# Kernel optimization log

Measured on AMD Instinct MI355X. Metric: run time of the kernel, lower is better.

The kernel has to match this reference:

```python
import jax, jax.numpy as jnp
import numpy as np

D = 64        # inner_feature_len (dim)
HID = 128     # hidden_channels of the edge MLP
NCONV = 2     # n_conv
STEPS = 3     # Set2Set processing_steps
NSEG = 128    # number of graphs in the batch


def setup_inputs() -> dict:
    key = jax.random.key(0)
    ks = jax.random.split(key, 30)
    N, E, FN, FE = 10000, 64000, 92, 41
    s = 0.05
    p = lambda i, shape: jax.random.normal(ks[i], shape, jnp.float32) * s
    return {
        "x": jax.random.normal(ks[0], (N, FN), jnp.float32),
        "edge_attr": jax.random.uniform(ks[1], (E, FE), dtype=jnp.float32),
        "lin0_w": p(2, (D, FN)), "lin0_b": p(3, (D,)),
        "nn1_w": p(4, (HID, FE)), "nn1_b": p(5, (HID,)),
        "nn2_w": p(6, (D * D, HID)), "nn2_b": p(7, (D * D,)),
        "root_w": p(8, (D, D)), "conv_b": p(9, (D,)),
        "gru_w_ih": p(10, (3 * D, D)), "gru_w_hh": p(11, (3 * D, D)),
        "gru_b_ih": p(12, (3 * D,)), "gru_b_hh": p(13, (3 * D,)),
        "lstm_w_ih": p(14, (4 * D, 2 * D)), "lstm_w_hh": p(15, (4 * D, D)),
        "lstm_b_ih": p(16, (4 * D,)), "lstm_b_hh": p(17, (4 * D,)),
        "lin1_w": p(18, (D, 2 * D)), "lin1_b": p(19, (D,)),
        "lin2_w": p(20, (1, D)), "lin2_b": p(21, (1,)),
        "edge_index": jax.random.randint(ks[22], (2, E), 0, N, dtype=jnp.int32),
        "batch": jnp.sort(jax.random.randint(ks[23], (N,), 0, NSEG, dtype=jnp.int32)),
    }


def _gru_step(m, h, w_ih, w_hh, b_ih, b_hh):
    # torch GRU gate order: r, z, n
    gi = m @ w_ih.T + b_ih
    gh = h @ w_hh.T + b_hh
    r = jax.nn.sigmoid(gi[:, :D] + gh[:, :D])
    z = jax.nn.sigmoid(gi[:, D:2 * D] + gh[:, D:2 * D])
    n = jnp.tanh(gi[:, 2 * D:] + r * gh[:, 2 * D:])
    return (1.0 - z) * n + z * h


def _forward(x, edge_attr, lin0_w, lin0_b, nn1_w, nn1_b, nn2_w, nn2_b, root_w, conv_b,
             gru_w_ih, gru_w_hh, gru_b_ih, gru_b_hh, lstm_w_ih, lstm_w_hh, lstm_b_ih,
             lstm_b_hh, lin1_w, lin1_b, lin2_w, lin2_b, edge_index, batch):
    N = x.shape[0]
    src, dst = edge_index[0], edge_index[1]

    # Edge-conditioned weight matrices: [E, D, D] (dominant intermediate)
    We = (jax.nn.relu(edge_attr @ nn1_w.T + nn1_b) @ nn2_w.T + nn2_b).reshape(-1, D, D)
    deg = jnp.clip(jax.ops.segment_sum(jnp.ones_like(src, jnp.float32), dst, num_segments=N), 1.0, None)

    out = jax.nn.relu(x @ lin0_w.T + lin0_b)   # [N, D]
    h = out                                     # GRU hidden (num_layers=1)
    for _ in range(NCONV):
        # NNConv: gather -> per-edge matmul -> scatter-mean, plus root transform + bias
        msg = jnp.einsum('ei,eio->eo', out[src], We)                 # [E, D]
        agg = jax.ops.segment_sum(msg, dst, num_segments=N) / deg[:, None]
        m = jax.nn.relu(agg + out @ root_w.T + conv_b)
        h = _gru_step(m, h, gru_w_ih, gru_w_hh, gru_b_ih, gru_b_hh)
        out = h

    # Set2Set pooling (LSTM-attention readout)
    q_star = jnp.zeros((NSEG, 2 * D), x.dtype)
    hl = jnp.zeros((NSEG, D), x.dtype)
    cl = jnp.zeros((NSEG, D), x.dtype)
    for _ in range(STEPS):
        g = q_star @ lstm_w_ih.T + lstm_b_ih + hl @ lstm_w_hh.T + lstm_b_hh
        i = jax.nn.sigmoid(g[:, :D])
        f = jax.nn.sigmoid(g[:, D:2 * D])
        gg = jnp.tanh(g[:, 2 * D:3 * D])
        o = jax.nn.sigmoid(g[:, 3 * D:])
        cl = f * cl + i * gg
        hl = o * jnp.tanh(cl)
        q = hl                                   # [NSEG, D]
        e = jnp.sum(out * q[batch], axis=-1)     # [N]
        mmax = jax.ops.segment_max(e, batch, num_segments=NSEG)
        a = jnp.exp(e - mmax[batch])
        denom = jax.ops.segment_sum(a, batch, num_segments=NSEG)
        a = a / denom[batch]
        r = jax.ops.segment_sum(a[:, None] * out, batch, num_segments=NSEG)  # [NSEG, D]
        q_star = jnp.concatenate([q, r], axis=1)

    y = jax.nn.relu(q_star @ lin1_w.T + lin1_b) @ lin2_w.T + lin2_b
    return y.reshape(-1)


def reference(x, edge_attr, lin0_w, lin0_b, nn1_w, nn1_b, nn2_w, nn2_b, root_w, conv_b,
              gru_w_ih, gru_w_hh, gru_b_ih, gru_b_hh, lstm_w_ih, lstm_w_hh, lstm_b_ih,
              lstm_b_hh, lin1_w, lin1_b, lin2_w, lin2_b, edge_index, batch):
    return _forward(x, edge_attr, lin0_w, lin0_b, nn1_w, nn1_b, nn2_w, nn2_b, root_w,
                    conv_b, gru_w_ih, gru_w_hh, gru_b_ih, gru_b_hh, lstm_w_ih, lstm_w_hh,
                    lstm_b_ih, lstm_b_hh, lin1_w, lin1_b, lin2_w, lin2_b, edge_index, batch)
```

## Files before the change

kernel.cpp:

```cpp
#include <hip/hip_runtime.h>
#include <hip/hip_bf16.h>
#include <math.h>

#define DD 64
#define HIDC 128
#define FN 92
#define FE 41
#define S2CAP 192

typedef unsigned short u16;
typedef short bf16x8 __attribute__((ext_vector_type(8)));
typedef float f32x4 __attribute__((ext_vector_type(4)));
typedef u16 u16x8 __attribute__((ext_vector_type(8)));

__device__ __forceinline__ float sigmoidf_(float x){ return 1.f/(1.f+expf(-x)); }

__device__ __forceinline__ u16 f2bf(float v){
  union { float f; unsigned u; } x; x.f = v;
  unsigned r = x.u + 0x7fff + ((x.u >> 16) & 1);
  return (u16)(r >> 16);
}
__device__ __forceinline__ float bf2f(u16 v){
  union { float f; unsigned u; } x; x.u = ((unsigned)v) << 16;
  return x.f;
}
__device__ __forceinline__ void split_bf(float v, u16& h, u16& l){
  h = f2bf(v); l = f2bf(v - bf2f(h));
}

__global__ void k_pack(const float* __restrict__ lin0_w, const float* __restrict__ nn1_w,
                       const float* __restrict__ root_w, const float* __restrict__ gwih,
                       const float* __restrict__ gwhh, const float* __restrict__ lwih,
                       const float* __restrict__ lwhh, const float* __restrict__ lin1_w,
                       float* __restrict__ lin0T, float* __restrict__ nn1T,
                       float* __restrict__ rootT, float* __restrict__ wihT,
                       float* __restrict__ whhT, float* __restrict__ lwihT,
                       float* __restrict__ lwhhT, float* __restrict__ lin1T)
{
  int idx = blockIdx.x*blockDim.x + threadIdx.x;
  if (idx < 92*64){ int k=idx/64, o=idx%64; lin0T[k*64+o] = lin0_w[o*92+k]; return; } idx -= 92*64;
  if (idx < 41*128){ int k=idx/128, h=idx%128; nn1T[k*128+h] = nn1_w[h*41+k]; return; } idx -= 41*128;
  if (idx < 64*64){ int i=idx/64, o=idx%64; rootT[i*64+o] = root_w[o*64+i]; return; } idx -= 64*64;
  if (idx < 64*192){ int i=idx/192, g=idx%192; wihT[i*192+g] = gwih[g*64+i]; return; } idx -= 64*192;
  if (idx < 64*192){ int i=idx/192, g=idx%192; whhT[i*192+g] = gwhh[g*64+i]; return; } idx -= 64*192;
  if (idx < 128*256){ int j=idx/256, t=idx%256; lwihT[j*256+t] = lwih[t*128+j]; return; } idx -= 128*256;
  if (idx < 64*256){ int j=idx/256, t=idx%256; lwhhT[j*256+t] = lwhh[t*64+j]; return; } idx -= 64*256;
  if (idx < 128*64){ int j=idx/64, t=idx%64; lin1T[j*64+t] = lin1_w[t*128+j]; return; }
}

__global__ void k_pack_b2(const float* __restrict__ nn2_w,
                          u16* __restrict__ BhT, u16* __restrict__ BlT){
  int idx = blockIdx.x*256 + threadIdx.x;
  if (idx >= 524288) return;
  int i  = idx & 63;
  int ho = (idx >> 6) & 4095;
  int c  = idx >> 18;
  int h = ho >> 6, o = ho & 63;
  float v = nn2_w[(size_t)(i*64+o)*128 + c*64 + h];
  u16 hi, lo; split_bf(v, hi, lo);
  BhT[idx] = hi; BlT[idx] = lo;
}

__global__ void k_pack_b1(const float* __restrict__ nn1_w,
                          u16* __restrict__ BT1h, u16* __restrict__ BT1l){
  int idx = blockIdx.x*256 + threadIdx.x;
  if (idx >= 8192) return;
  int h = idx >> 6, k = idx & 63;
  float v = (k < FE) ? nn1_w[(size_t)h*FE + k] : 0.f;
  u16 hi, lo; split_bf(v, hi, lo);
  BT1h[idx] = hi; BT1l[idx] = lo;
}

__global__ void k_split_ea(const float* __restrict__ ea, const int* __restrict__ sortedE,
                           u16* __restrict__ eaH, u16* __restrict__ eaL, int E){
  int idx = blockIdx.x*256 + threadIdx.x;
  if (idx >= E*64) return;
  int ew = idx >> 6, k = idx & 63;
  int e = sortedE[ew];
  float v = (k < FE) ? ea[(size_t)e*FE + k] : 0.f;
  u16 hi, lo; split_bf(v, hi, lo);
  eaH[idx] = hi; eaL[idx] = lo;
}

__global__ __launch_bounds__(256) void k_node_mlp(const float* __restrict__ x,
    const float* __restrict__ lin0T, const float* __restrict__ lin0_b,
    const float* __restrict__ nn2_b,
    float* __restrict__ out, u16* __restrict__ outH, u16* __restrict__ outL,
    float* __restrict__ bterm, int N)
{
  __shared__ float xs[16][FN];
  const int w = threadIdx.x>>6, o = threadIdx.x&63;
  const int nb = blockIdx.x*16 + w*4;
  for (int idx = o; idx < 4*FN; idx += 64){
    int j = idx/FN, k = idx%FN;
    int n = nb + j;
    xs[w*4+j][k] = (n<N) ? x[(size_t)n*FN + k] : 0.f;
  }
  float acc[4];
  float bv = lin0_b[o];
  #pragma unroll
  for (int j=0;j<4;j++) acc[j] = bv;
  for (int k=0;k<FN;k++){
    float lw = lin0T[k*64+o];
    #pragma unroll
    for (int j=0;j<4;j++) acc[j] = fmaf(xs[w*4+j][k], lw, acc[j]);
  }
  float v[4];
  #pragma unroll
  for (int j=0;j<4;j++){
    v[j] = fmaxf(acc[j], 0.f);
    int n = nb + j;
    if (n < N){
      out[(size_t)n*64+o] = v[j];
      u16 hi, lo; split_bf(v[j], hi, lo);
      outH[(size_t)n*64+o] = hi;
      outL[(size_t)n*64+o] = lo;
    }
  }
  float bt[4] = {0.f,0.f,0.f,0.f};
  for (int i=0;i<64;i++){
    float wnb = nn2_b[i*64+o];
    #pragma unroll
    for (int j=0;j<4;j++) bt[j] = fmaf(__shfl(v[j], i, 64), wnb, bt[j]);
  }
  #pragma unroll
  for (int j=0;j<4;j++){
    int n = nb + j;
    if (n < N) bterm[(size_t)n*64+o] = bt[j];
  }
}

__global__ void k_count(const int* __restrict__ dst, const int* __restrict__ src,
                        float* __restrict__ deg, int* __restrict__ scnt, int E){
  int e = blockIdx.x*blockDim.x + threadIdx.x;
  if (e < E){
    atomicAdd(&deg[dst[e]], 1.f);
    atomicAdd(&scnt[src[e]], 1);
  }
}

__global__ void k_scan1(const int* __restrict__ cnt, int* __restrict__ excl,
                        int* __restrict__ bsum, int N){
  __shared__ int buf[256];
  int i = blockIdx.x*256 + threadIdx.x;
  int v = (i<N) ? cnt[i] : 0;
  buf[threadIdx.x] = v;
  __syncthreads();
  #pragma unroll
  for (int off=1; off<256; off<<=1){
    int t = (threadIdx.x>=off) ? buf[threadIdx.x-off] : 0;
    __syncthreads();
    buf[threadIdx.x] += t;
    __syncthreads();
  }
  if (i<N) excl[i] = buf[threadIdx.x] - v;
  if (threadIdx.x==255) bsum[blockIdx.x] = buf[255];
}
__global__ void k_scan2(int* __restrict__ bsum, int nb){
  __shared__ int buf[256];
  int v = (threadIdx.x<nb) ? bsum[threadIdx.x] : 0;
  buf[threadIdx.x] = v;
  __syncthreads();
  #pragma unroll
  for (int off=1; off<256; off<<=1){
    int t = (threadIdx.x>=off) ? buf[threadIdx.x-off] : 0;
    __syncthreads();
    buf[threadIdx.x] += t;
    __syncthreads();
  }
  if (threadIdx.x<nb) bsum[threadIdx.x] = buf[threadIdx.x] - v;
}
__global__ void k_scan3(int* __restrict__ starts, int* __restrict__ cursor,
                        const int* __restrict__ bsum, int N, int E){
  int i = blockIdx.x*256 + threadIdx.x;
  if (i<N){
    int s = starts[i] + bsum[blockIdx.x];
    starts[i] = s;
    cursor[i] = s;
  }
  if (i==0) starts[N] = E;
}

__global__ void k_sort(const int* __restrict__ src, const int* __restrict__ dst,
                       int* __restrict__ cursor, int* __restrict__ sortedE,
                       int* __restrict__ dstS, int E){
  int e = blockIdx.x*256 + threadIdx.x;
  if (e < E){
    int s = src[e];
    int p = atomicAdd(&cursor[s], 1);
    sortedE[p] = e;
    dstS[p] = dst[e];
  }
}

__global__ __launch_bounds__(256,3) void k_edge_mlp_mfma(
    const u16* __restrict__ eaH, const u16* __restrict__ eaL,
    const u16* __restrict__ BT1h, const u16* __restrict__ BT1l,
    const float* __restrict__ nn1_b, float* __restrict__ hidden, int E)
{
  const int lane = threadIdx.x & 63;
  const int wave = threadIdx.x >> 6;
  const int row  = lane & 15;
  const int quad = lane >> 4;
  const int m0 = blockIdx.x*128 + (wave>>1)*64;
  const int n0 = (wave&1)*64;

  bf16x8 AH0[4], AH1[4], AL0[4], AL1[4];
  #pragma unroll
  for (int p=0;p<4;p++){
    int ar = min(m0 + p*16 + row, E-1);
    const u16* aH = eaH + (size_t)ar*64 + quad*8;
    const u16* aL = eaL + (size_t)ar*64 + quad*8;
    AH0[p] = *(const bf16x8*)(aH);
    AH1[p] = *(const bf16x8*)(aH + 32);
    AL0[p] = *(const bf16x8*)(aL);
    AL1[p] = *(const bf16x8*)(aL + 32);
  }
  #pragma unroll
  for (int tb=0;tb<4;tb++){
    const u16* bH = BT1h + (size_t)(n0 + tb*16 + row)*64 + quad*8;
    const u16* bL = BT1l + (size_t)(n0 + tb*16 + row)*64 + quad*8;
    bf16x8 bh0 = *(const bf16x8*)(bH);
    bf16x8 bh1 = *(const bf16x8*)(bH + 32);
    bf16x8 bl0 = *(const bf16x8*)(bL);
    bf16x8 bl1 = *(const bf16x8*)(bL + 32);
    float4 bias;
    {
      int nb = n0 + tb*16 + quad*4;
      bias.x = nn1_b[nb+0]; bias.y = nn1_b[nb+1];
      bias.z = nn1_b[nb+2]; bias.w = nn1_b[nb+3];
    }
    #pragma unroll
    for (int ta=0;ta<4;ta++){
      f32x4 a = {0.f,0.f,0.f,0.f};
      a = __builtin_amdgcn_mfma_f32_16x16x32_bf16(bh0, AH0[ta], a, 0,0,0);
      a = __builtin_amdgcn_mfma_f32_16x16x32_bf16(bh1, AH1[ta], a, 0,0,0);
      a = __builtin_amdgcn_mfma_f32_16x16x32_bf16(bl0, AH0[ta], a, 0,0,0);
      a = __builtin_amdgcn_mfma_f32_16x16x32_bf16(bl1, AH1[ta], a, 0,0,0);
      a = __builtin_amdgcn_mfma_f32_16x16x32_bf16(bh0, AL0[ta], a, 0,0,0);
      a = __builtin_amdgcn_mfma_f32_16x16x32_bf16(bh1, AL1[ta], a, 0,0,0);
      int m = m0 + ta*16 + row;
      if (m < E){
        float4 v;
        v.x = fmaxf(a[0]+bias.x, 0.f); v.y = fmaxf(a[1]+bias.y, 0.f);
        v.z = fmaxf(a[2]+bias.z, 0.f); v.w = fmaxf(a[3]+bias.w, 0.f);
        *(float4*)(hidden + (size_t)m*128 + n0 + tb*16 + quad*4) = v;
      }
    }
  }
}

__global__ __launch_bounds__(256,3) void k_qgemm_mfma(
    const u16* __restrict__ Ah, const u16* __restrict__ Al,
    const u16* __restrict__ BhT, const u16* __restrict__ BlT,
    u16* __restrict__ C, int M, int cbase)
{
  const int lane = threadIdx.x & 63;
  const int wave = threadIdx.x >> 6;
  const int row  = lane & 15;
  const int quad = lane >> 4;
  const int m0 = blockIdx.y * 64;
  const int col = cbase + blockIdx.x * 256 + wave * 64;
  const int chunk = col >> 12;
  const int n0 = col & 4095;
  const u16* Bh = BhT + (size_t)chunk*262144;
  const u16* Bl = BlT + (size_t)chunk*262144;

  bf16x8 AH0[4], AH1[4], AL0[4], AL1[4];
  #pragma unroll
  for (int p=0;p<4;p++){
    int ar = min(m0 + p*16 + row, M-1);
    const u16* aH = Ah + (size_t)ar*64 + quad*8;
    const u16* aL = Al + (size_t)ar*64 + quad*8;
    AH0[p] = *(const bf16x8*)(aH);
    AH1[p] = *(const bf16x8*)(aH + 32);
    AL0[p] = *(const bf16x8*)(aL);
    AL1[p] = *(const bf16x8*)(aL + 32);
  }

  f32x4 acc[4][4];
  #pragma unroll
  for (int ta=0;ta<4;ta++)
    #pragma unroll
    for (int tb=0;tb<4;tb++)
      acc[ta][tb] = (f32x4){0.f,0.f,0.f,0.f};

  #pragma unroll
  for (int tb=0;tb<4;tb++){
    const u16* bH = Bh + (size_t)(n0 + tb*16 + row)*64 + quad*8;
    const u16* bL = Bl + (size_t)(n0 + tb*16 + row)*64 + quad*8;
    bf16x8 bh0 = *(const bf16x8*)(bH);
    bf16x8 bh1 = *(const bf16x8*)(bH + 32);
    bf16x8 bl0 = *(const bf16x8*)(bL);
    bf16x8 bl1 = *(const bf16x8*)(bL + 32);
    #pragma unroll
    for (int ta=0;ta<4;ta++){
      f32x4 a = acc[ta][tb];
      a = __builtin_amdgcn_mfma_f32_16x16x32_bf16(bh0, AH0[ta], a, 0,0,0);
      a = __builtin_amdgcn_mfma_f32_16x16x32_bf16(bh1, AH1[ta], a, 0,0,0);
      a = __builtin_amdgcn_mfma_f32_16x16x32_bf16(bl0, AH0[ta], a, 0,0,0);
      a = __builtin_amdgcn_mfma_f32_16x16x32_bf16(bl1, AH1[ta], a, 0,0,0);
      a = __builtin_amdgcn_mfma_f32_16x16x32_bf16(bh0, AL0[ta], a, 0,0,0);
      a = __builtin_amdgcn_mfma_f32_16x16x32_bf16(bh1, AL1[ta], a, 0,0,0);
      acc[ta][tb] = a;
    }
  }

  const int cbl = (col - cbase) >> 6;
  #pragma unroll
  for (int ta=0;ta<4;ta++){
    int m = m0 + ta*16 + row;
    if (m >= M) continue;
    u16* dst = C + ((size_t)cbl*M + m)*64 + quad*8;
    #pragma unroll
    for (int p=0;p<2;p++){
      f32x4 aa = acc[ta][2*p];
      f32x4 ab = acc[ta][2*p+1];
      u16x8 v;
      v[0]=f2bf(aa[0]); v[1]=f2bf(aa[1]); v[2]=f2bf(aa[2]); v[3]=f2bf(aa[3]);
      v[4]=f2bf(ab[0]); v[5]=f2bf(ab[1]); v[6]=f2bf(ab[2]); v[7]=f2bf(ab[3]);
      *(u16x8*)(dst + p*32) = v;
    }
  }
}

__global__ __launch_bounds__(256) void k_edge_gather(const u16* __restrict__ Q,
    const float* __restrict__ hidden, int h0, int cb0, int addbt,
    const float* __restrict__ bterm, const int* __restrict__ starts,
    const int* __restrict__ dstS, float* __restrict__ agg, int N)
{
  __shared__ float hs[4][64];
  __shared__ float red[4][64];
  const int wv = threadIdx.x>>6, lane = threadIdx.x&63;
  const int n = blockIdx.x*4 + wv;
  if (n >= N) return;
  const int e0 = starts[n], e1 = starts[n+1];
  if (e0 >= e1) return;
  const int sg = lane>>4, oq = lane&15;
  const int posb = ((oq>>3)<<5) + ((oq&3)<<3) + (((oq>>2)&1)<<2);
  const u16* qp = Q + ((size_t)(cb0+sg)*N + n)*64 + posb;
  const size_t jstride = (size_t)N*256;
  ushort4 qreg[16];
  #pragma unroll
  for (int j=0;j<16;j++) qreg[j] = *(const ushort4*)(qp + (size_t)j*jstride);
  const float bt = addbt ? bterm[(size_t)n*64 + lane] : 0.f;

  float hvN = hidden[(size_t)e0*128 + h0 + lane];
  int   dN  = dstS[e0];
  for (int e=e0; e<e1; ++e){
    const float hv = hvN;
    const int   d  = dN;
    if (e+1 < e1){
      hvN = hidden[(size_t)(e+1)*128 + h0 + lane];
      dN  = dstS[e+1];
    }
    hs[wv][lane] = hv;
    float a0=0.f,a1=0.f,a2=0.f,a3=0.f;
    #pragma unroll
    for (int j=0;j<16;j++){
      float h4 = hs[wv][j*4+sg];
      a0 = fmaf(h4, bf2f(qreg[j].x), a0);
      a1 = fmaf(h4, bf2f(qreg[j].y), a1);
      a2 = fmaf(h4, bf2f(qreg[j].z), a2);
      a3 = fmaf(h4, bf2f(qreg[j].w), a3);
    }
    a0 += __shfl_xor(a0,16); a0 += __shfl_xor(a0,32);
    a1 += __shfl_xor(a1,16); a1 += __shfl_xor(a1,32);
    a2 += __shfl_xor(a2,16); a2 += __shfl_xor(a2,32);
    a3 += __shfl_xor(a3,16); a3 += __shfl_xor(a3,32);
    if (lane < 16){
      float4 r; r.x=a0; r.y=a1; r.z=a2; r.w=a3;
      *(float4*)&red[wv][lane*4] = r;
    }
    atomicAdd(&agg[(size_t)d*64 + lane], bt + red[wv][lane]);
  }
}

__global__ __launch_bounds__(256) void k_node_update(const float* __restrict__ outOld,
    const float* __restrict__ agg, const float* __restrict__ deg,
    const float* __restrict__ rootT, const float* __restrict__ conv_b,
    const float* __restrict__ wihT, const float* __restrict__ whhT,
    const float* __restrict__ b_ih, const float* __restrict__ b_hh,
    const float* __restrict__ nn2_b,
    float* __restrict__ outNew, u16* __restrict__ outH, u16* __restrict__ outL,
    float* __restrict__ bterm, int N)
{
  __shared__ float hs[16][64];
  __shared__ float ms[16][64];
  const int w = threadIdx.x>>6, o = threadIdx.x&63;
  const int nb = blockIdx.x*16 + w*4;
  float h[4];
  #pragma unroll
  for (int j=0;j<4;j++){
    int n = nb+j;
    h[j] = (n<N) ? outOld[(size_t)n*64+o] : 0.f;
    hs[w*4+j][o] = h[j];
  }
  float root[4] = {0.f,0.f,0.f,0.f};
  for (int i=0;i<64;i++){
    float rw = rootT[i*64+o];
    #pragma unroll
    for (int j=0;j<4;j++) root[j] = fmaf(hs[w*4+j][i], rw, root[j]);
  }
  float cb = conv_b[o];
  float m[4];
  #pragma unroll
  for (int j=0;j<4;j++){
    int n = nb+j;
    float d = (n<N) ? fmaxf(deg[n], 1.f) : 1.f;
    float a = (n<N) ? agg[(size_t)n*64+o]/d : 0.f;
    m[j] = fmaxf(a + root[j] + cb, 0.f);
    ms[w*4+j][o] = m[j];
  }
  float gir[4],giz[4],gin[4],ghr[4],ghz[4],ghn[4];
  float bir=b_ih[o], biz=b_ih[64+o], bin=b_ih[128+o];
  float bhr=b_hh[o], bhz=b_hh[64+o], bhn=b_hh[128+o];
  #pragma unroll
  for (int j=0;j<4;j++){
    gir[j]=bir; giz[j]=biz; gin[j]=bin;
    ghr[j]=bhr; ghz[j]=bhz; ghn[j]=bhn;
  }
  for (int i=0;i<64;i++){
    float wr=wihT[i*192+o], wz=wihT[i*192+64+o], wn=wihT[i*192+128+o];
    float vr=whhT[i*192+o], vz=whhT[i*192+64+o], vn=whhT[i*192+128+o];
    #pragma unroll
    for (int j=0;j<4;j++){
      float mi = ms[w*4+j][i], hi = hs[w*4+j][i];
      gir[j]=fmaf(mi,wr,gir[j]); giz[j]=fmaf(mi,wz,giz[j]); gin[j]=fmaf(mi,wn,gin[j]);
      ghr[j]=fmaf(hi,vr,ghr[j]); ghz[j]=fmaf(hi,vz,ghz[j]); ghn[j]=fmaf(hi,vn,ghn[j]);
    }
  }
  float v[4];
  #pragma unroll
  for (int j=0;j<4;j++){
    float r = sigmoidf_(gir[j]+ghr[j]);
    float z = sigmoidf_(giz[j]+ghz[j]);
    float nn = tanhf(gin[j] + r*ghn[j]);
    v[j] = (1.f-z)*nn + z*h[j];
    int n = nb+j;
    if (n<N){
      outNew[(size_t)n*64+o] = v[j];
      u16 hi16, lo16; split_bf(v[j], hi16, lo16);
      outH[(size_t)n*64+o] = hi16;
      outL[(size_t)n*64+o] = lo16;
    }
  }
  float bt[4] = {0.f,0.f,0.f,0.f};
  for (int i=0;i<64;i++){
    float wnb = nn2_b[i*64+o];
    #pragma unroll
    for (int j=0;j<4;j++) bt[j] = fmaf(__shfl(v[j], i, 64), wnb, bt[j]);
  }
  #pragma unroll
  for (int j=0;j<4;j++){
    int n = nb+j;
    if (n<N) bterm[(size_t)n*64+o] = bt[j];
  }
}

__global__ __launch_bounds__(256) void k_set2set(const float* __restrict__ out,
    const int* __restrict__ batch, int N,
    const float* __restrict__ lwihT, const float* __restrict__ lwhhT,
    const float* __restrict__ b_ih, const float* __restrict__ b_hh,
    const float* __restrict__ lin1T, const float* __restrict__ lin1_b,
    const float* __restrict__ lin2_w, const float* __restrict__ lin2_b,
    float* __restrict__ y)
{
  __shared__ float X[S2CAP][65];
  __shared__ float earr[S2CAP];
  __shared__ float qstar[128], hl[64], cl[64], g[256];
  __shared__ float rpart[4][64], spart[4], redm[4], zs[64];
  __shared__ int sb[2];
  const int tid = threadIdx.x;
  const int b = blockIdx.x;
  const int wid = tid>>6, lane = tid&63;
  if (tid < 128) qstar[tid] = 0.f;
  if (tid < 64){ hl[tid]=0.f; cl[tid]=0.f; }
  if (tid == 0){
    int lo=0, hi=N;
    while (lo<hi){ int mid=(lo+hi)>>1; if (batch[mid] < b) lo=mid+1; else hi=mid; }
    sb[0]=lo;
    int lo2=lo, hi2=N;
    while (lo2<hi2){ int mid=(lo2+hi2)>>1; if (batch[mid] < b+1) lo2=mid+1; else hi2=mid; }
    sb[1]=lo2;
  }
  __syncthreads();
  const int nlo = sb[0], nhi = sb[1], nn = nhi - nlo;
  const bool single = (nn <= S2CAP);
  if (single){
    for (int idx = tid; idx < nn*64; idx += 256){
      X[idx>>6][idx&63] = out[(size_t)(nlo + (idx>>6))*64 + (idx&63)];
    }
  }
  __syncthreads();

  for (int step=0; step<3; step++){
    float gs = b_ih[tid] + b_hh[tid];
    for (int j=0;j<128;j++) gs = fmaf(qstar[j], lwihT[j*256+tid], gs);
    for (int j=0;j<64;j++)  gs = fmaf(hl[j],    lwhhT[j*256+tid], gs);
    g[tid] = gs;
    __syncthreads();
    if (tid < 64){
      float ig = sigmoidf_(g[tid]);
      float fg = sigmoidf_(g[64+tid]);
      float gg = tanhf(g[128+tid]);
      float og = sigmoidf_(g[192+tid]);
      float c = fg*cl[tid] + ig*gg;
      cl[tid] = c;
      hl[tid] = og*tanhf(c);
    }
    __syncthreads();

    if (single){
      float lm = -INFINITY;
      for (int n = tid; n < nn; n += 256){
        float acc = 0.f;
        #pragma unroll 8
        for (int d=0; d<64; d++) acc = fmaf(X[n][d], hl[d], acc);
        earr[n] = acc;
        lm = fmaxf(lm, acc);
      }
      lm = fmaxf(lm, __shfl_xor(lm,1));  lm = fmaxf(lm, __shfl_xor(lm,2));
      lm = fmaxf(lm, __shfl_xor(lm,4));  lm = fmaxf(lm, __shfl_xor(lm,8));
      lm = fmaxf(lm, __shfl_xor(lm,16)); lm = fmaxf(lm, __shfl_xor(lm,32));
      if (lane==0) redm[wid] = lm;
      __syncthreads();
      if (tid==0) redm[0] = fmaxf(fmaxf(redm[0],redm[1]), fmaxf(redm[2],redm[3]));
      __syncthreads();
      const float gmax = redm[0];
      float ls = 0.f;
      for (int n = tid; n < nn; n += 256){
        float a = expf(earr[n] - gmax);
        earr[n] = a;
        ls += a;
      }
      ls += __shfl_xor(ls,1);  ls += __shfl_xor(ls,2);  ls += __shfl_xor(ls,4);
      ls += __shfl_xor(ls,8);  ls += __shfl_xor(ls,16); ls += __shfl_xor(ls,32);
      if (lane==0) spart[wid] = ls;
      __syncthreads();
      float racc = 0.f;
      for (int n = wid; n < nn; n += 4) racc = fmaf(earr[n], X[n][lane], racc);
      rpart[wid][lane] = racc;
      __syncthreads();
      if (tid < 64){
        float r = rpart[0][tid]+rpart[1][tid]+rpart[2][tid]+rpart[3][tid];
        float s = spart[0]+spart[1]+spart[2]+spart[3];
        qstar[tid] = hl[tid];
        qstar[64+tid] = (nn>0) ? r/s : 0.f;
      }
      __syncthreads();
    } else {
      float qv = hl[lane];
      float lm = -INFINITY;
      for (int n = nlo + wid; n < nhi; n += 4){
        float p = out[(size_t)n*64 + lane]*qv;
        p += __shfl_xor(p,1); p += __shfl_xor(p,2); p += __shfl_xor(p,4);
        p += __shfl_xor(p,8); p += __shfl_xor(p,16); p += __shfl_xor(p,32);
        lm = fmaxf(lm, p);
      }
      if (lane==0) redm[wid] = lm;
      __syncthreads();
      if (tid==0) redm[0] = fmaxf(fmaxf(redm[0],redm[1]), fmaxf(redm[2],redm[3]));
      __syncthreads();
      float gmax = redm[0];
      float sw = 0.f, racc = 0.f;
      for (int n = nlo + wid; n < nhi; n += 4){
        float ol = out[(size_t)n*64 + lane];
        float p = ol*qv;
        p += __shfl_xor(p,1); p += __shfl_xor(p,2); p += __shfl_xor(p,4);
        p += __shfl_xor(p,8); p += __shfl_xor(p,16); p += __shfl_xor(p,32);
        float a = expf(p - gmax);
        sw += a;
        racc = fmaf(a, ol, racc);
      }
      rpart[wid][lane] = racc;
      if (lane==0) spart[wid] = sw;
      __syncthreads();
      if (tid < 64){
        float r = rpart[0][tid]+rpart[1][tid]+rpart[2][tid]+rpart[3][tid];
        float s = spart[0]+spart[1]+spart[2]+spart[3];
        qstar[tid] = hl[tid];
        qstar[64+tid] = (nn>0) ? r/s : 0.f;
      }
      __syncthreads();
    }
  }
  if (tid < 64){
    float acc = lin1_b[tid];
    for (int j=0;j<128;j++) acc = fmaf(qstar[j], lin1T[j*64+tid], acc);
    zs[tid] = fmaxf(acc, 0.f);
  }
  __syncthreads();
  if (tid < 64){
    float v = zs[lane]*lin2_w[lane];
    v += __shfl_xor(v,1); v += __shfl_xor(v,2); v += __shfl_xor(v,4);
    v += __shfl_xor(v,8); v += __shfl_xor(v,16); v += __shfl_xor(v,32);
    if (lane==0) y[b] = v + lin2_b[0];
  }
}

extern "C" void kernel_launch(void* const* d_in, const int* in_sizes, int n_in,
                              void* d_out, int out_size, void* d_ws, size_t ws_size,
                              hipStream_t stream)
{
  const float* x      = (const float*)d_in[0];
  const float* eattr  = (const float*)d_in[1];
  const float* lin0_w = (const float*)d_in[2];
  const float* lin0_b = (const float*)d_in[3];
  const float* nn1_w  = (const float*)d_in[4];
  const float* nn1_b  = (const float*)d_in[5];
  const float* nn2_w  = (const float*)d_in[6];
  const float* nn2_b  = (const float*)d_in[7];
  const float* root_w = (const float*)d_in[8];
  const float* conv_b = (const float*)d_in[9];
  const float* gwih   = (const float*)d_in[10];
  const float* gwhh   = (const float*)d_in[11];
  const float* gbih   = (const float*)d_in[12];
  const float* gbhh   = (const float*)d_in[13];
  const float* lwih   = (const float*)d_in[14];
  const float* lwhh   = (const float*)d_in[15];
  const float* lbih   = (const float*)d_in[16];
  const float* lbhh   = (const float*)d_in[17];
  const float* lin1_w = (const float*)d_in[18];
  const float* lin1_b = (const float*)d_in[19];
  const float* lin2_w = (const float*)d_in[20];
  const float* lin2_b = (const float*)d_in[21];
  const int*   eidx   = (const int*)d_in[22];
  const int*   batch  = (const int*)d_in[23];

  const int N = in_sizes[0]/FN;
  const int E = in_sizes[1]/FE;
  const int* srcI = eidx;
  const int* dstI = eidx + E;

  char* w = (char*)d_ws;
  size_t off = 0;
  auto alloc = [&](size_t bytes)->char* {
    char* p = w + off;
    off = (off + bytes + 255) & ~(size_t)255;
    return p;
  };
  float* degw  = (float*)alloc((size_t)N*4);
  int*   scnt  = (int*)alloc((size_t)N*4);
  int*   starts= (int*)alloc((size_t)(N+1)*4);
  int*   cursor= (int*)alloc((size_t)N*4);
  int*   bsum  = (int*)alloc((size_t)256*4);
  int*   sortedE=(int*)alloc((size_t)E*4);
  int*   dstS  = (int*)alloc((size_t)E*4);
  float* outA  = (float*)alloc((size_t)N*64*4);
  float* outB  = (float*)alloc((size_t)N*64*4);
  u16*   outAH = (u16*)alloc((size_t)N*64*2);
  u16*   outAL = (u16*)alloc((size_t)N*64*2);
  u16*   outBH = (u16*)alloc((size_t)N*64*2);
  u16*   outBL = (u16*)alloc((size_t)N*64*2);
  float* agg   = (float*)alloc((size_t)N*64*4);
  float* bterm = (float*)alloc((size_t)N*64*4);
  float* hidden= (float*)alloc((size_t)E*128*4);
  u16*   B2hT  = (u16*)alloc((size_t)524288*2);
  u16*   B2lT  = (u16*)alloc((size_t)524288*2);
  u16*   BT1h  = (u16*)alloc((size_t)8192*2);
  u16*   BT1l  = (u16*)alloc((size_t)8192*2);
  float* lin0T = (float*)alloc((size_t)92*64*4);
  float* nn1T  = (float*)alloc((size_t)41*128*4);
  float* rootT = (float*)alloc((size_t)64*64*4);
  float* wihT  = (float*)alloc((size_t)64*192*4);
  float* whhT  = (float*)alloc((size_t)64*192*4);
  float* lwihT = (float*)alloc((size_t)128*256*4);
  float* lwhhT = (float*)alloc((size_t)64*256*4);
  float* lin1T = (float*)alloc((size_t)128*64*4);

  size_t qbig = (size_t)N*8192*2;
  size_t qsmall = (size_t)N*4096*2;
  bool merged = (ws_size - off) >= (qbig + 512);
  u16* Q = (u16*)alloc(merged ? qbig : qsmall);
  u16* eaH = (u16*)Q;
  u16* eaL = eaH + (size_t)E*64;

  const int NB = (N+255)/256;

  hipMemsetAsync(degw, 0, (size_t)N*4, stream);
  hipMemsetAsync(scnt, 0, (size_t)N*4, stream);
  k_pack<<<(97152+255)/256, 256, 0, stream>>>(lin0_w, nn1_w, root_w, gwih, gwhh,
      lwih, lwhh, lin1_w, lin0T, nn1T, rootT, wihT, whhT, lwihT, lwhhT, lin1T);
  k_pack_b2<<<524288/256, 256, 0, stream>>>(nn2_w, B2hT, B2lT);
  k_pack_b1<<<8192/256, 256, 0, stream>>>(nn1_w, BT1h, BT1l);
  k_node_mlp<<<(N+15)/16, 256, 0, stream>>>(x, lin0T, lin0_b, nn2_b, outA, outAH, outAL, bterm, N);
  k_count<<<(E+255)/256, 256, 0, stream>>>(dstI, srcI, degw, scnt, E);
  k_scan1<<<NB, 256, 0, stream>>>(scnt, starts, bsum, N);
  k_scan2<<<1, 256, 0, stream>>>(bsum, NB);
  k_scan3<<<NB, 256, 0, stream>>>(starts, cursor, bsum, N, E);
  k_sort<<<(E+255)/256, 256, 0, stream>>>(srcI, dstI, cursor, sortedE, dstS, E);
  k_split_ea<<<((size_t)E*64+255)/256, 256, 0, stream>>>(eattr, sortedE, eaH, eaL, E);
  k_edge_mlp_mfma<<<(E+127)/128, 256, 0, stream>>>(eaH, eaL, BT1h, BT1l, nn1_b, hidden, E);

  float* cur = outA; float* nxt = outB;
  u16* curH = outAH; u16* curL = outAL;
  u16* nxtH = outBH; u16* nxtL = outBL;
  const int gatherG = (N+3)/4;
  for (int conv=0; conv<2; conv++){
    hipMemsetAsync(agg, 0, (size_t)N*64*4, stream);
    if (merged){
      k_qgemm_mfma<<<dim3(32,(N+63)/64), 256, 0, stream>>>(curH, curL, B2hT, B2lT, Q, N, 0);
      k_edge_gather<<<gatherG, 256, 0, stream>>>(Q, hidden, 0,  0,  1, bterm, starts, dstS, agg, N);
      k_edge_gather<<<gatherG, 256, 0, stream>>>(Q, hidden, 64, 64, 0, bterm, starts, dstS, agg, N);
    } else {
      for (int c=0; c<2; c++){
        k_qgemm_mfma<<<dim3(16,(N+63)/64), 256, 0, stream>>>(curH, curL, B2hT, B2lT, Q, N, c*4096);
        k_edge_gather<<<gatherG, 256, 0, stream>>>(Q, hidden, c*64, 0, (c==0)?1:0, bterm, starts, dstS, agg, N);
      }
    }
    k_node_update<<<(N+15)/16, 256, 0, stream>>>(cur, agg, degw, rootT, conv_b,
        wihT, whhT, gbih, gbhh, nn2_b, nxt, nxtH, nxtL, bterm, N);
    float* t = cur; cur = nxt; nxt = t;
    u16* th = curH; curH = nxtH; nxtH = th;
    u16* tl = curL; curL = nxtL; nxtL = tl;
  }

  k_set2set<<<128, 256, 0, stream>>>(cur, batch, N, lwihT, lwhhT, lbih, lbhh,
      lin1T, lin1_b, lin2_w, lin2_b, (float*)d_out);
}
```

Baseline: 587.6 us.

## Store Q node-major and always split the edge GEMM into two half passes

The Q intermediate is now laid out node-major, so each node owns a contiguous 4096-element row, and the gather reads it with small strides instead of N-scaled strides. The merged single-GEMM path that needed a double-size Q buffer is removed. Each conv now always runs two qgemm+gather passes over half the hidden channels, which keeps Q at half size and likely inside cache. The cost is an extra GEMM launch per conv when the workspace would have allowed the merged path, and the qgemm stores are now strided by 4096 per row.

```diff
diff --git a/kernel.cpp b/kernel.cpp
--- a/kernel.cpp
+++ b/kernel.cpp
@@ -253,18 +253,14 @@
 __global__ __launch_bounds__(256,3) void k_qgemm_mfma(
     const u16* __restrict__ Ah, const u16* __restrict__ Al,
     const u16* __restrict__ BhT, const u16* __restrict__ BlT,
-    u16* __restrict__ C, int M, int cbase)
+    u16* __restrict__ C, int M)
 {
   const int lane = threadIdx.x & 63;
   const int wave = threadIdx.x >> 6;
   const int row  = lane & 15;
   const int quad = lane >> 4;
   const int m0 = blockIdx.y * 64;
-  const int col = cbase + blockIdx.x * 256 + wave * 64;
-  const int chunk = col >> 12;
-  const int n0 = col & 4095;
-  const u16* Bh = BhT + (size_t)chunk*262144;
-  const u16* Bl = BlT + (size_t)chunk*262144;
+  const int n0 = blockIdx.x * 256 + wave * 64;
 
   bf16x8 AH0[4], AH1[4], AL0[4], AL1[4];
   #pragma unroll
@@ -287,8 +283,8 @@
 
   #pragma unroll
   for (int tb=0;tb<4;tb++){
-    const u16* bH = Bh + (size_t)(n0 + tb*16 + row)*64 + quad*8;
-    const u16* bL = Bl + (size_t)(n0 + tb*16 + row)*64 + quad*8;
+    const u16* bH = BhT + (size_t)(n0 + tb*16 + row)*64 + quad*8;
+    const u16* bL = BlT + (size_t)(n0 + tb*16 + row)*64 + quad*8;
     bf16x8 bh0 = *(const bf16x8*)(bH);
     bf16x8 bh1 = *(const bf16x8*)(bH + 32);
     bf16x8 bl0 = *(const bf16x8*)(bL);
@@ -306,12 +302,11 @@
     }
   }
 
-  const int cbl = (col - cbase) >> 6;
   #pragma unroll
   for (int ta=0;ta<4;ta++){
     int m = m0 + ta*16 + row;
     if (m >= M) continue;
-    u16* dst = C + ((size_t)cbl*M + m)*64 + quad*8;
+    u16* dst = C + (size_t)m*4096 + n0 + quad*8;
     #pragma unroll
     for (int p=0;p<2;p++){
       f32x4 aa = acc[ta][2*p];
@@ -324,8 +319,9 @@
   }
 }
 
+template<int PASS>
 __global__ __launch_bounds__(256) void k_edge_gather(const u16* __restrict__ Q,
-    const float* __restrict__ hidden, int h0, int cb0, int addbt,
+    const float* __restrict__ hidden, int h0,
     const float* __restrict__ bterm, const int* __restrict__ starts,
     const int* __restrict__ dstS, float* __restrict__ agg, int N)
 {
@@ -338,12 +334,11 @@
   if (e0 >= e1) return;
   const int sg = lane>>4, oq = lane&15;
   const int posb = ((oq>>3)<<5) + ((oq&3)<<3) + (((oq>>2)&1)<<2);
-  const u16* qp = Q + ((size_t)(cb0+sg)*N + n)*64 + posb;
-  const size_t jstride = (size_t)N*256;
+  const u16* qp = Q + (size_t)n*4096 + sg*64 + posb;
   ushort4 qreg[16];
   #pragma unroll
-  for (int j=0;j<16;j++) qreg[j] = *(const ushort4*)(qp + (size_t)j*jstride);
-  const float bt = addbt ? bterm[(size_t)n*64 + lane] : 0.f;
+  for (int j=0;j<16;j++) qreg[j] = *(const ushort4*)(qp + j*256);
+  const float bt = (PASS==0) ? bterm[(size_t)n*64 + lane] : 0.f;
 
   float hvN = hidden[(size_t)e0*128 + h0 + lane];
   int   dN  = dstS[e0];
@@ -668,11 +663,7 @@
   float* lwihT = (float*)alloc((size_t)128*256*4);
   float* lwhhT = (float*)alloc((size_t)64*256*4);
   float* lin1T = (float*)alloc((size_t)128*64*4);
-
-  size_t qbig = (size_t)N*8192*2;
-  size_t qsmall = (size_t)N*4096*2;
-  bool merged = (ws_size - off) >= (qbig + 512);
-  u16* Q = (u16*)alloc(merged ? qbig : qsmall);
+  u16*   Q     = (u16*)alloc((size_t)N*4096*2);
   u16* eaH = (u16*)Q;
   u16* eaL = eaH + (size_t)E*64;
 
@@ -696,19 +687,14 @@
   float* cur = outA; float* nxt = outB;
   u16* curH = outAH; u16* curL = outAL;
   u16* nxtH = outBH; u16* nxtL = outBL;
+  const dim3 qgrid(16, (N+63)/64);
   const int gatherG = (N+3)/4;
   for (int conv=0; conv<2; conv++){
     hipMemsetAsync(agg, 0, (size_t)N*64*4, stream);
-    if (merged){
-      k_qgemm_mfma<<<dim3(32,(N+63)/64), 256, 0, stream>>>(curH, curL, B2hT, B2lT, Q, N, 0);
-      k_edge_gather<<<gatherG, 256, 0, stream>>>(Q, hidden, 0,  0,  1, bterm, starts, dstS, agg, N);
-      k_edge_gather<<<gatherG, 256, 0, stream>>>(Q, hidden, 64, 64, 0, bterm, starts, dstS, agg, N);
-    } else {
-      for (int c=0; c<2; c++){
-        k_qgemm_mfma<<<dim3(16,(N+63)/64), 256, 0, stream>>>(curH, curL, B2hT, B2lT, Q, N, c*4096);
-        k_edge_gather<<<gatherG, 256, 0, stream>>>(Q, hidden, c*64, 0, (c==0)?1:0, bterm, starts, dstS, agg, N);
-      }
-    }
+    k_qgemm_mfma<<<qgrid, 256, 0, stream>>>(curH, curL, B2hT, B2lT, Q, N);
+    k_edge_gather<0><<<gatherG, 256, 0, stream>>>(Q, hidden, 0, bterm, starts, dstS, agg, N);
+    k_qgemm_mfma<<<qgrid, 256, 0, stream>>>(curH, curL, B2hT + 262144, B2lT + 262144, Q, N);
+    k_edge_gather<1><<<gatherG, 256, 0, stream>>>(Q, hidden, 64, bterm, starts, dstS, agg, N);
     k_node_update<<<(N+15)/16, 256, 0, stream>>>(cur, agg, degw, rootT, conv_b,
         wihT, whhT, gbih, gbhh, nn2_b, nxt, nxtH, nxtL, bterm, N);
     float* t = cur; cur = nxt; nxt = t;
```

After: 582.4 us. About the same (-0.9%).
